# Optimization experiments

Measured on AMD Instinct MI355X. Metric: run time of the kernel, lower is better.

Reference implementation:

```python
import jax, jax.numpy as jnp
import numpy as np
import math

B, S, D, H = 2, 2048, 1024, 16
DK = D // H


def setup_inputs() -> dict:
    key = jax.random.key(0)
    ks = jax.random.split(key, 12)
    std = 1.0 / math.sqrt(D)
    inp = {
        "query": jax.random.normal(ks[0], (B, S, D), jnp.float32),
        "key": jax.random.normal(ks[1], (B, S, D), jnp.float32),
        "value": jax.random.normal(ks[2], (B, S, D), jnp.float32),
        # causal mask, broadcast over batch and heads
        "mask": jnp.tril(jnp.ones((S, S), jnp.int32))[None, None, :, :],
        # nn.Linear weights are [out_features, in_features]
        "Wq": jax.random.uniform(ks[3], (D, D), jnp.float32, -std, std),
        "bq": jax.random.uniform(ks[4], (D,), jnp.float32, -std, std),
        "Wk": jax.random.uniform(ks[5], (D, D), jnp.float32, -std, std),
        "bk": jax.random.uniform(ks[6], (D,), jnp.float32, -std, std),
        "Wv": jax.random.uniform(ks[7], (D, D), jnp.float32, -std, std),
        "bv": jax.random.uniform(ks[8], (D,), jnp.float32, -std, std),
        "Wo": jax.random.uniform(ks[9], (D, D), jnp.float32, -std, std),
        "bo": jax.random.uniform(ks[10], (D,), jnp.float32, -std, std),
    }
    return inp


def reference(query, key, value, mask, Wq, bq, Wk, bk, Wv, bv, Wo, bo):
    q = query @ Wq.T + bq  # [B,S,D]
    k = key @ Wk.T + bk
    v = value @ Wv.T + bv
    # Faithful to the original: a raw view (reshape), NOT a head-transpose split.
    q = q.reshape(B, H, S, DK)
    k = k.reshape(B, H, S, DK)
    v = v.reshape(B, H, S, DK)
    scores = jnp.einsum("bhqd,bhkd->bhqk", q, k) / math.sqrt(DK)
    scores = jnp.where(mask == 0, jnp.float32(-1e9), scores)
    weights = jax.nn.softmax(scores, axis=-1)
    # dropout(p=0.1) is identity in eval mode
    context = jnp.einsum("bhqk,bhkd->bhqd", weights, v)
    context = context.transpose(0, 2, 1, 3).reshape(B, S, D)
    return context @ Wo.T + bo
```

## Files before the change

### kernel.cpp

```cpp
#include <hip/hip_runtime.h>
#include <hip/hip_bf16.h>

#define BB 2
#define SS 2048
#define DD 1024
#define HH 16
#define DKK 64

typedef __attribute__((ext_vector_type(4))) float  f32x4;
typedef __attribute__((ext_vector_type(8))) short  s16x8;
typedef __attribute__((ext_vector_type(4))) short  s16x4;
typedef __attribute__((ext_vector_type(4))) float  fvec4;

__device__ __forceinline__ short f2bs(float f) {
    union { __hip_bfloat16 b; short s; } u;
    u.b = __float2bfloat16(f);
    return u.s;
}

__device__ __forceinline__ void gload_lds16(const short* g, short* l) {
    __builtin_amdgcn_global_load_lds((const __attribute__((address_space(1))) void*)g,
                                     (__attribute__((address_space(3))) void*)l, 16, 0, 0);
}

__global__ __launch_bounds__(256) void cvt_all(
    const float* __restrict__ q,  const float* __restrict__ k,  const float* __restrict__ v,
    const float* __restrict__ wq, const float* __restrict__ wk, const float* __restrict__ wv,
    const float* __restrict__ wo,
    short* __restrict__ qo,  short* __restrict__ ko,  short* __restrict__ vo,
    short* __restrict__ wqo, short* __restrict__ wko, short* __restrict__ wvo,
    short* __restrict__ woo)
{
    const float* src; short* dst; int n;
    switch (blockIdx.y) {
        case 0: src = q;  dst = qo;  n = BB * SS * DD; break;
        case 1: src = k;  dst = ko;  n = BB * SS * DD; break;
        case 2: src = v;  dst = vo;  n = BB * SS * DD; break;
        case 3: src = wq; dst = wqo; n = DD * DD; break;
        case 4: src = wk; dst = wko; n = DD * DD; break;
        case 5: src = wv; dst = wvo; n = DD * DD; break;
        default: src = wo; dst = woo; n = DD * DD; break;
    }
    int i = (blockIdx.x * 256 + threadIdx.x) * 8;
    const int stride = gridDim.x * 256 * 8;
    for (; i < n; i += stride) {
        fvec4 a = *(const fvec4*)&src[i];
        fvec4 b = *(const fvec4*)&src[i + 4];
        s16x8 o;
        o[0] = f2bs(a[0]); o[1] = f2bs(a[1]); o[2] = f2bs(a[2]); o[3] = f2bs(a[3]);
        o[4] = f2bs(b[0]); o[5] = f2bs(b[1]); o[6] = f2bs(b[2]); o[7] = f2bs(b[3]);
        *(s16x8*)&dst[i] = o;
    }
}

template<bool OUTF32>
__global__ __launch_bounds__(256) void gemm_nt_v2(
    const short* __restrict__ A0, const short* __restrict__ A1, const short* __restrict__ A2,
    const short* __restrict__ B0, const short* __restrict__ B1, const short* __restrict__ B2,
    const float* __restrict__ c0, const float* __restrict__ c1, const float* __restrict__ c2,
    void* __restrict__ O0, void* __restrict__ O1, void* __restrict__ O2,
    float os0, float os1, float os2,
    int ko0, int ko1, int ko2,
    int ppx, int NY, int KL, int N, int K)
{
    const int d   = blockIdx.x;
    const int xcd = d & 7;
    const int s   = d >> 3;
    const int x   = s & 7;
    const int pl  = s >> 3;
    const int panel = xcd * ppx + pl;
    const int y   = panel % NY;
    const int z   = panel / NY;

    const short* A    = z == 0 ? A0 : (z == 1 ? A1 : A2);
    const short* Bw   = z == 0 ? B0 : (z == 1 ? B1 : B2);
    const float* bias = z == 0 ? c0 : (z == 1 ? c1 : c2);
    void* Cp          = z == 0 ? O0 : (z == 1 ? O1 : O2);
    const float oscale = z == 0 ? os0 : (z == 1 ? os1 : os2);
    const int koff     = z == 0 ? ko0 : (z == 1 ? ko1 : ko2);

    __shared__ short As[128][64];
    __shared__ short Bs[128][64];

    const int tid  = threadIdx.x;
    const int lane = tid & 63;
    const int wid  = tid >> 6;
    const int r16  = lane & 15;
    const int g    = lane >> 4;
    const int m0   = y * 128;
    const int n0   = x * 128;
    const int wr   = (wid >> 1) * 64;
    const int wc   = (wid & 1) * 64;
    const int srow8 = lane >> 3;
    const int c8    = lane & 7;

    f32x4 acc[4][4];
#pragma unroll
    for (int mi = 0; mi < 4; ++mi)
#pragma unroll
        for (int ni = 0; ni < 4; ++ni) acc[mi][ni] = (f32x4){0.f, 0.f, 0.f, 0.f};

    const int csrc = (c8 ^ srow8) * 8;
    const int nk = KL >> 6;
#pragma unroll 1
    for (int kt = 0; kt < nk; ++kt) {
        const int k0 = koff + kt * 64;
        if (kt) __syncthreads();
#pragma unroll
        for (int q = 0; q < 4; ++q) {
            const int r = wid * 32 + q * 8 + srow8;
            gload_lds16(&A[(size_t)(m0 + r) * K + k0 + csrc], &As[wid * 32 + q * 8][0]);
        }
#pragma unroll
        for (int q = 0; q < 4; ++q) {
            const int r = wid * 32 + q * 8 + srow8;
            gload_lds16(&Bw[(size_t)(n0 + r) * K + k0 + csrc], &Bs[wid * 32 + q * 8][0]);
        }
        __syncthreads();

#pragma unroll
        for (int kk = 0; kk < 2; ++kk) {
            s16x8 af[4], bf[4];
#pragma unroll
            for (int mi = 0; mi < 4; ++mi) {
                const int row = wr + mi * 16 + r16;
                af[mi] = *(const s16x8*)&As[row][((kk * 4 + g) ^ (row & 7)) * 8];
            }
#pragma unroll
            for (int ni = 0; ni < 4; ++ni) {
                const int row = wc + ni * 16 + r16;
                bf[ni] = *(const s16x8*)&Bs[row][((kk * 4 + g) ^ (row & 7)) * 8];
            }
#pragma unroll
            for (int mi = 0; mi < 4; ++mi)
#pragma unroll
                for (int ni = 0; ni < 4; ++ni)
                    acc[mi][ni] = __builtin_amdgcn_mfma_f32_16x16x32_bf16(
                        af[mi], bf[ni], acc[mi][ni], 0, 0, 0);
        }
    }

#pragma unroll
    for (int ni = 0; ni < 4; ++ni) {
        const int col = n0 + wc + ni * 16 + r16;
        const float bv = bias ? bias[col] : 0.f;
#pragma unroll
        for (int mi = 0; mi < 4; ++mi) {
#pragma unroll
            for (int r = 0; r < 4; ++r) {
                const int row = m0 + wr + mi * 16 + g * 4 + r;
                const float vv = (acc[mi][ni][r] + bv) * oscale;
                if constexpr (OUTF32)
                    ((float*)Cp)[(size_t)row * N + col] = vv;
                else
                    ((short*)Cp)[(size_t)row * N + col] = f2bs(vv);
            }
        }
    }
}

__global__ __launch_bounds__(256) void combine_o(
    const float* __restrict__ P0, const float* __restrict__ P1,
    const float* __restrict__ bo, float* __restrict__ out)
{
    const int n = BB * SS * DD;
    int i = (blockIdx.x * 256 + threadIdx.x) * 8;
    const int stride = gridDim.x * 256 * 8;
    for (; i < n; i += stride) {
        fvec4 a0 = *(const fvec4*)&P0[i];
        fvec4 a1 = *(const fvec4*)&P0[i + 4];
        fvec4 b0 = *(const fvec4*)&P1[i];
        fvec4 b1 = *(const fvec4*)&P1[i + 4];
        fvec4 c0 = *(const fvec4*)&bo[i & (DD - 1)];
        fvec4 c1 = *(const fvec4*)&bo[(i + 4) & (DD - 1)];
        fvec4 o0 = a0 + b0 + c0;
        fvec4 o1 = a1 + b1 + c1;
        *(fvec4*)&out[i] = o0;
        *(fvec4*)&out[i + 4] = o1;
    }
}

__global__ __launch_bounds__(256) void mha_transpose_v(
    const short* __restrict__ vp, short* __restrict__ vT)
{
    const int st = blockIdx.x;
    const int bh = blockIdx.y;
    const short* src = vp + (size_t)bh * SS * DKK;
    short*       dst = vT + (size_t)bh * SS * DKK;
    const int tid = threadIdx.x;
#pragma unroll
    for (int i = 0; i < 2; ++i) {
        const int c  = tid + i * 256;
        const int dk = c >> 3;
        const int sc = c & 7;
        const int s0 = st * 64 + sc * 8;
        s16x8 v;
#pragma unroll
        for (int j = 0; j < 8; ++j) v[j] = src[(size_t)(s0 + j) * DKK + dk];
        *(s16x8*)&dst[(size_t)dk * SS + s0] = v;
    }
}

__global__ __launch_bounds__(256, 2) void mha_attn(
    const short* __restrict__ qp, const short* __restrict__ kp,
    const short* __restrict__ vT, short* __restrict__ ctx)
{
    __shared__ short Ks[64][64];
    __shared__ short Vs[64][64];
    __shared__ short P[4][16][72];

    const int tid  = threadIdx.x;
    const int wid  = tid >> 6;
    const int lane = tid & 63;
    const int r16  = lane & 15;
    const int g    = lane >> 4;

    const int bh  = blockIdx.x;
    const int bxp = blockIdx.y;
    const int b   = bh >> 4;
    const int h   = bh & 15;

    const short* Qh = qp + (size_t)bh * SS * DKK;
    const short* Kh = kp + (size_t)bh * SS * DKK;
    const short* Vh = vT + (size_t)bh * SS * DKK;

    const int srow = lane >> 3;
    const int r0   = wid * 16;

#pragma unroll 1
    for (int t = 0; t < 2; ++t) {
        const int grp = t ? (31 - bxp) : bxp;
        const int qr0 = grp * 64 + wid * 16;
        const int nkt = grp + 1;

        const s16x8 qf0 = *(const s16x8*)&Qh[(size_t)(qr0 + r16) * DKK + g * 8];
        const s16x8 qf1 = *(const s16x8*)&Qh[(size_t)(qr0 + r16) * DKK + 32 + g * 8];

        f32x4 po[4];
#pragma unroll
        for (int i = 0; i < 4; ++i) po[i] = (f32x4){0.f, 0.f, 0.f, 0.f};
        float l_[4] = {0.f, 0.f, 0.f, 0.f};

#pragma unroll 1
        for (int j = 0; j < nkt; ++j) {
            const int k0 = j * 64;
            __syncthreads();
            {
                const int rowA = r0 + srow;
                const int rowB = rowA + 8;
                const int cA = (((lane & 7) ^ (rowA & 7)) & 7) * 8;
                const int cB = (((lane & 7) ^ (rowB & 7)) & 7) * 8;
                gload_lds16(&Kh[(size_t)(k0 + rowA) * DKK + cA], &Ks[r0][0]);
                gload_lds16(&Kh[(size_t)(k0 + rowB) * DKK + cB], &Ks[r0 + 8][0]);
                gload_lds16(&Vh[(size_t)rowA * SS + k0 + cA], &Vs[r0][0]);
                gload_lds16(&Vh[(size_t)rowB * SS + k0 + cB], &Vs[r0 + 8][0]);
            }
            __syncthreads();

            f32x4 sc[4];
            __builtin_amdgcn_s_setprio(1);
#pragma unroll
            for (int cg = 0; cg < 4; ++cg) {
                const int R  = cg * 16 + r16;
                const int sw = R & 7;
                const s16x8 kf0 = *(const s16x8*)&Ks[R][((g ^ sw) & 7) * 8];
                const s16x8 kf1 = *(const s16x8*)&Ks[R][(((4 + g) ^ sw) & 7) * 8];
                f32x4 tt = (f32x4){0.f, 0.f, 0.f, 0.f};
                tt = __builtin_amdgcn_mfma_f32_16x16x32_bf16(qf0, kf0, tt, 0, 0, 0);
                tt = __builtin_amdgcn_mfma_f32_16x16x32_bf16(qf1, kf1, tt, 0, 0, 0);
                sc[cg] = tt;
            }
            __builtin_amdgcn_s_setprio(0);

            if (j == nkt - 1) {
#pragma unroll
                for (int cg = 0; cg < 4; ++cg)
#pragma unroll
                    for (int r = 0; r < 4; ++r)
                        if (k0 + cg * 16 + r16 > qr0 + g * 4 + r) sc[cg][r] = -1e9f;
            }
#pragma unroll
            for (int cg = 0; cg < 4; ++cg)
#pragma unroll
                for (int r = 0; r < 4; ++r) {
                    const float p = __expf(sc[cg][r]);
                    l_[r] += p;
                    P[wid][g * 4 + r][cg * 16 + r16] = f2bs(p);
                }
            const s16x8 pf0 = *(const s16x8*)&P[wid][r16][g * 8];
            const s16x8 pf1 = *(const s16x8*)&P[wid][r16][32 + g * 8];

            __builtin_amdgcn_s_setprio(1);
#pragma unroll
            for (int dg = 0; dg < 4; ++dg) {
                const int Rv = dg * 16 + r16;
                const int sw = Rv & 7;
                const s16x8 vf0 = *(const s16x8*)&Vs[Rv][((g ^ sw) & 7) * 8];
                const s16x8 vf1 = *(const s16x8*)&Vs[Rv][(((4 + g) ^ sw) & 7) * 8];
                po[dg] = __builtin_amdgcn_mfma_f32_16x16x32_bf16(pf0, vf0, po[dg], 0, 0, 0);
                po[dg] = __builtin_amdgcn_mfma_f32_16x16x32_bf16(pf1, vf1, po[dg], 0, 0, 0);
            }
            __builtin_amdgcn_s_setprio(0);
        }

#pragma unroll
        for (int r = 0; r < 4; ++r) {
#pragma unroll
            for (int off = 1; off < 16; off <<= 1)
                l_[r] += __shfl_xor(l_[r], off);
        }
#pragma unroll
        for (int dg = 0; dg < 4; ++dg)
#pragma unroll
            for (int r = 0; r < 4; ++r) {
                const int srw = qr0 + g * 4 + r;
                const float v = po[dg][r] * __builtin_amdgcn_rcpf(l_[r]);
                ctx[((size_t)(b * SS + srw)) * DD + h * 64 + dg * 16 + r16] = f2bs(v);
            }
    }
}

extern "C" void kernel_launch(void* const* d_in, const int* in_sizes, int n_in,
                              void* d_out, int out_size, void* d_ws, size_t ws_size,
                              hipStream_t stream) {
    const float* query = (const float*)d_in[0];
    const float* key   = (const float*)d_in[1];
    const float* value = (const float*)d_in[2];
    const float* Wq = (const float*)d_in[4];
    const float* bq = (const float*)d_in[5];
    const float* Wk = (const float*)d_in[6];
    const float* bk = (const float*)d_in[7];
    const float* Wv = (const float*)d_in[8];
    const float* bv = (const float*)d_in[9];
    const float* Wo = (const float*)d_in[10];
    const float* bo = (const float*)d_in[11];
    float* out = (float*)d_out;

    const size_t elems = (size_t)BB * SS * DD;
    const size_t wel   = (size_t)DD * DD;
    short* qx  = (short*)d_ws;
    short* kx  = qx + elems;
    short* vx  = kx + elems;
    short* wqx = vx + elems;
    short* wkx = wqx + wel;
    short* wvx = wkx + wel;
    short* wox = wvx + wel;
    short* qp  = wox + wel;
    short* kp  = qp + elems;
    short* vp  = kp + elems;
    short* vT  = qx;
    short* ctx = vx;
    float* P0  = (float*)qx;
    float* P1  = (float*)qp;

    const int M = BB * SS;

    cvt_all<<<dim3(1024, 7), 256, 0, stream>>>(query, key, value, Wq, Wk, Wv, Wo,
                                               qx, kx, vx, wqx, wkx, wvx, wox);
    gemm_nt_v2<false><<<dim3(768), 256, 0, stream>>>(
        qx, kx, vx, wqx, wkx, wvx, bq, bk, bv, qp, kp, vp,
        0.125f, 1.0f, 1.0f, 0, 0, 0, 12, 32, 1024, DD, DD);
    mha_transpose_v<<<dim3(SS / 64, BB * HH), 256, 0, stream>>>(vp, vT);
    mha_attn<<<dim3(BB * HH, 16), 256, 0, stream>>>(qp, kp, vT, ctx);
    gemm_nt_v2<true><<<dim3(512), 256, 0, stream>>>(
        ctx, ctx, ctx, wox, wox, wox, nullptr, nullptr, nullptr,
        (void*)P0, (void*)P1, (void*)P1,
        1.0f, 1.0f, 1.0f, 0, 512, 512, 8, 32, 512, DD, DD);
    combine_o<<<dim3(2048), 256, 0, stream>>>(P0, P1, bo, out);
}
```

Before: 128.5 us.

## Double-buffer K/V tiles in attention and drop split-K output projection

The attention kernel now stages the next K/V tile into a second LDS buffer while the current tile is computed, using explicit vmcnt waits and raw barriers in place of the load-then-sync pattern. The output projection moves from a split-K GEMM with fp32 partials plus a combine kernel to a single full-K GEMM with a 128x64 tile that adds the bias and writes the output directly. This removes one kernel launch and the traffic for the fp32 partials, and it hides global load latency in attention. The cost is twice the LDS for K/V, which can lower occupancy, and hand-written waitcnt logic that depends on how many loads are in flight.

```diff
diff --git a/kernel.cpp b/kernel.cpp
--- a/kernel.cpp
+++ b/kernel.cpp
@@ -53,21 +53,20 @@
     }
 }
 
-template<bool OUTF32>
+template<int BN, int NXSH, bool OUTF32>
 __global__ __launch_bounds__(256) void gemm_nt_v2(
     const short* __restrict__ A0, const short* __restrict__ A1, const short* __restrict__ A2,
     const short* __restrict__ B0, const short* __restrict__ B1, const short* __restrict__ B2,
     const float* __restrict__ c0, const float* __restrict__ c1, const float* __restrict__ c2,
     void* __restrict__ O0, void* __restrict__ O1, void* __restrict__ O2,
     float os0, float os1, float os2,
-    int ko0, int ko1, int ko2,
     int ppx, int NY, int KL, int N, int K)
 {
     const int d   = blockIdx.x;
     const int xcd = d & 7;
     const int s   = d >> 3;
-    const int x   = s & 7;
-    const int pl  = s >> 3;
+    const int x   = s & ((1 << NXSH) - 1);
+    const int pl  = s >> NXSH;
     const int panel = xcd * ppx + pl;
     const int y   = panel % NY;
     const int z   = panel / NY;
@@ -77,10 +76,9 @@
     const float* bias = z == 0 ? c0 : (z == 1 ? c1 : c2);
     void* Cp          = z == 0 ? O0 : (z == 1 ? O1 : O2);
     const float oscale = z == 0 ? os0 : (z == 1 ? os1 : os2);
-    const int koff     = z == 0 ? ko0 : (z == 1 ? ko1 : ko2);
 
     __shared__ short As[128][64];
-    __shared__ short Bs[128][64];
+    __shared__ short Bs[BN][64];
 
     const int tid  = threadIdx.x;
     const int lane = tid & 63;
@@ -88,23 +86,25 @@
     const int r16  = lane & 15;
     const int g    = lane >> 4;
     const int m0   = y * 128;
-    const int n0   = x * 128;
+    const int n0   = x * BN;
+    constexpr int MR = 4;
+    constexpr int NR = BN / 32;
     const int wr   = (wid >> 1) * 64;
-    const int wc   = (wid & 1) * 64;
+    const int wc   = (wid & 1) * (BN / 2);
     const int srow8 = lane >> 3;
     const int c8    = lane & 7;
 
-    f32x4 acc[4][4];
-#pragma unroll
-    for (int mi = 0; mi < 4; ++mi)
-#pragma unroll
-        for (int ni = 0; ni < 4; ++ni) acc[mi][ni] = (f32x4){0.f, 0.f, 0.f, 0.f};
+    f32x4 acc[MR][NR];
+#pragma unroll
+    for (int mi = 0; mi < MR; ++mi)
+#pragma unroll
+        for (int ni = 0; ni < NR; ++ni) acc[mi][ni] = (f32x4){0.f, 0.f, 0.f, 0.f};
 
     const int csrc = (c8 ^ srow8) * 8;
     const int nk = KL >> 6;
 #pragma unroll 1
     for (int kt = 0; kt < nk; ++kt) {
-        const int k0 = koff + kt * 64;
+        const int k0 = kt * 64;
         if (kt) __syncthreads();
 #pragma unroll
         for (int q = 0; q < 4; ++q) {
@@ -112,40 +112,40 @@
             gload_lds16(&A[(size_t)(m0 + r) * K + k0 + csrc], &As[wid * 32 + q * 8][0]);
         }
 #pragma unroll
-        for (int q = 0; q < 4; ++q) {
-            const int r = wid * 32 + q * 8 + srow8;
-            gload_lds16(&Bw[(size_t)(n0 + r) * K + k0 + csrc], &Bs[wid * 32 + q * 8][0]);
+        for (int q = 0; q < BN / 32; ++q) {
+            const int r = wid * (BN / 4) + q * 8 + srow8;
+            gload_lds16(&Bw[(size_t)(n0 + r) * K + k0 + csrc], &Bs[wid * (BN / 4) + q * 8][0]);
         }
         __syncthreads();
 
 #pragma unroll
         for (int kk = 0; kk < 2; ++kk) {
-            s16x8 af[4], bf[4];
-#pragma unroll
-            for (int mi = 0; mi < 4; ++mi) {
+            s16x8 af[MR], bf[NR];
+#pragma unroll
+            for (int mi = 0; mi < MR; ++mi) {
                 const int row = wr + mi * 16 + r16;
                 af[mi] = *(const s16x8*)&As[row][((kk * 4 + g) ^ (row & 7)) * 8];
             }
 #pragma unroll
-            for (int ni = 0; ni < 4; ++ni) {
+            for (int ni = 0; ni < NR; ++ni) {
                 const int row = wc + ni * 16 + r16;
                 bf[ni] = *(const s16x8*)&Bs[row][((kk * 4 + g) ^ (row & 7)) * 8];
             }
 #pragma unroll
-            for (int mi = 0; mi < 4; ++mi)
-#pragma unroll
-                for (int ni = 0; ni < 4; ++ni)
+            for (int mi = 0; mi < MR; ++mi)
+#pragma unroll
+                for (int ni = 0; ni < NR; ++ni)
                     acc[mi][ni] = __builtin_amdgcn_mfma_f32_16x16x32_bf16(
                         af[mi], bf[ni], acc[mi][ni], 0, 0, 0);
         }
     }
 
 #pragma unroll
-    for (int ni = 0; ni < 4; ++ni) {
+    for (int ni = 0; ni < NR; ++ni) {
         const int col = n0 + wc + ni * 16 + r16;
         const float bv = bias ? bias[col] : 0.f;
 #pragma unroll
-        for (int mi = 0; mi < 4; ++mi) {
+        for (int mi = 0; mi < MR; ++mi) {
 #pragma unroll
             for (int r = 0; r < 4; ++r) {
                 const int row = m0 + wr + mi * 16 + g * 4 + r;
@@ -156,27 +156,6 @@
                     ((short*)Cp)[(size_t)row * N + col] = f2bs(vv);
             }
         }
-    }
-}
-
-__global__ __launch_bounds__(256) void combine_o(
-    const float* __restrict__ P0, const float* __restrict__ P1,
-    const float* __restrict__ bo, float* __restrict__ out)
-{
-    const int n = BB * SS * DD;
-    int i = (blockIdx.x * 256 + threadIdx.x) * 8;
-    const int stride = gridDim.x * 256 * 8;
-    for (; i < n; i += stride) {
-        fvec4 a0 = *(const fvec4*)&P0[i];
-        fvec4 a1 = *(const fvec4*)&P0[i + 4];
-        fvec4 b0 = *(const fvec4*)&P1[i];
-        fvec4 b1 = *(const fvec4*)&P1[i + 4];
-        fvec4 c0 = *(const fvec4*)&bo[i & (DD - 1)];
-        fvec4 c1 = *(const fvec4*)&bo[(i + 4) & (DD - 1)];
-        fvec4 o0 = a0 + b0 + c0;
-        fvec4 o1 = a1 + b1 + c1;
-        *(fvec4*)&out[i] = o0;
-        *(fvec4*)&out[i + 4] = o1;
     }
 }
 
@@ -205,8 +184,8 @@
     const short* __restrict__ qp, const short* __restrict__ kp,
     const short* __restrict__ vT, short* __restrict__ ctx)
 {
-    __shared__ short Ks[64][64];
-    __shared__ short Vs[64][64];
+    __shared__ short Ks[2][64][64];
+    __shared__ short Vs[2][64][64];
     __shared__ short P[4][16][72];
 
     const int tid  = threadIdx.x;
@@ -225,7 +204,18 @@
     const short* Vh = vT + (size_t)bh * SS * DKK;
 
     const int srow = lane >> 3;
+    const int csw  = (((lane & 7) ^ srow) & 7) * 8;
     const int r0   = wid * 16;
+
+    auto STAGE = [&](int buf, int j) {
+        const int k0 = j * 64;
+        const int rA = r0 + srow;
+        const int rB = rA + 8;
+        gload_lds16(&Kh[(size_t)(k0 + rA) * DKK + csw], &Ks[buf][r0][0]);
+        gload_lds16(&Kh[(size_t)(k0 + rB) * DKK + csw], &Ks[buf][r0 + 8][0]);
+        gload_lds16(&Vh[(size_t)rA * SS + k0 + csw],    &Vs[buf][r0][0]);
+        gload_lds16(&Vh[(size_t)rB * SS + k0 + csw],    &Vs[buf][r0 + 8][0]);
+    };
 
 #pragma unroll 1
     for (int t = 0; t < 2; ++t) {
@@ -241,21 +231,20 @@
         for (int i = 0; i < 4; ++i) po[i] = (f32x4){0.f, 0.f, 0.f, 0.f};
         float l_[4] = {0.f, 0.f, 0.f, 0.f};
 
+        STAGE(0, 0);
+
 #pragma unroll 1
         for (int j = 0; j < nkt; ++j) {
+            const int cur = j & 1;
             const int k0 = j * 64;
-            __syncthreads();
-            {
-                const int rowA = r0 + srow;
-                const int rowB = rowA + 8;
-                const int cA = (((lane & 7) ^ (rowA & 7)) & 7) * 8;
-                const int cB = (((lane & 7) ^ (rowB & 7)) & 7) * 8;
-                gload_lds16(&Kh[(size_t)(k0 + rowA) * DKK + cA], &Ks[r0][0]);
-                gload_lds16(&Kh[(size_t)(k0 + rowB) * DKK + cB], &Ks[r0 + 8][0]);
-                gload_lds16(&Vh[(size_t)rowA * SS + k0 + cA], &Vs[r0][0]);
-                gload_lds16(&Vh[(size_t)rowB * SS + k0 + cB], &Vs[r0 + 8][0]);
-            }
-            __syncthreads();
+            if (j + 1 < nkt) {
+                STAGE(cur ^ 1, j + 1);
+                asm volatile("s_waitcnt vmcnt(4)" ::: "memory");
+            } else {
+                asm volatile("s_waitcnt vmcnt(0)" ::: "memory");
+            }
+            __builtin_amdgcn_s_barrier();
+            __builtin_amdgcn_sched_barrier(0);
 
             f32x4 sc[4];
             __builtin_amdgcn_s_setprio(1);
@@ -263,8 +252,8 @@
             for (int cg = 0; cg < 4; ++cg) {
                 const int R  = cg * 16 + r16;
                 const int sw = R & 7;
-                const s16x8 kf0 = *(const s16x8*)&Ks[R][((g ^ sw) & 7) * 8];
-                const s16x8 kf1 = *(const s16x8*)&Ks[R][(((4 + g) ^ sw) & 7) * 8];
+                const s16x8 kf0 = *(const s16x8*)&Ks[cur][R][((g ^ sw) & 7) * 8];
+                const s16x8 kf1 = *(const s16x8*)&Ks[cur][R][(((4 + g) ^ sw) & 7) * 8];
                 f32x4 tt = (f32x4){0.f, 0.f, 0.f, 0.f};
                 tt = __builtin_amdgcn_mfma_f32_16x16x32_bf16(qf0, kf0, tt, 0, 0, 0);
                 tt = __builtin_amdgcn_mfma_f32_16x16x32_bf16(qf1, kf1, tt, 0, 0, 0);
@@ -295,12 +284,16 @@
             for (int dg = 0; dg < 4; ++dg) {
                 const int Rv = dg * 16 + r16;
                 const int sw = Rv & 7;
-                const s16x8 vf0 = *(const s16x8*)&Vs[Rv][((g ^ sw) & 7) * 8];
-                const s16x8 vf1 = *(const s16x8*)&Vs[Rv][(((4 + g) ^ sw) & 7) * 8];
+                const s16x8 vf0 = *(const s16x8*)&Vs[cur][Rv][((g ^ sw) & 7) * 8];
+                const s16x8 vf1 = *(const s16x8*)&Vs[cur][Rv][(((4 + g) ^ sw) & 7) * 8];
                 po[dg] = __builtin_amdgcn_mfma_f32_16x16x32_bf16(pf0, vf0, po[dg], 0, 0, 0);
                 po[dg] = __builtin_amdgcn_mfma_f32_16x16x32_bf16(pf1, vf1, po[dg], 0, 0, 0);
             }
             __builtin_amdgcn_s_setprio(0);
+
+            __builtin_amdgcn_sched_barrier(0);
+            asm volatile("s_waitcnt lgkmcnt(0)" ::: "memory");
+            __builtin_amdgcn_s_barrier();
         }
 
 #pragma unroll
@@ -350,21 +343,15 @@
     short* vp  = kp + elems;
     short* vT  = qx;
     short* ctx = vx;
-    float* P0  = (float*)qx;
-    float* P1  = (float*)qp;
-
-    const int M = BB * SS;
 
     cvt_all<<<dim3(1024, 7), 256, 0, stream>>>(query, key, value, Wq, Wk, Wv, Wo,
                                                qx, kx, vx, wqx, wkx, wvx, wox);
-    gemm_nt_v2<false><<<dim3(768), 256, 0, stream>>>(
+    gemm_nt_v2<128, 3, false><<<dim3(768), 256, 0, stream>>>(
         qx, kx, vx, wqx, wkx, wvx, bq, bk, bv, qp, kp, vp,
-        0.125f, 1.0f, 1.0f, 0, 0, 0, 12, 32, 1024, DD, DD);
+        0.125f, 1.0f, 1.0f, 12, 32, 1024, DD, DD);
     mha_transpose_v<<<dim3(SS / 64, BB * HH), 256, 0, stream>>>(vp, vT);
     mha_attn<<<dim3(BB * HH, 16), 256, 0, stream>>>(qp, kp, vT, ctx);
-    gemm_nt_v2<true><<<dim3(512), 256, 0, stream>>>(
-        ctx, ctx, ctx, wox, wox, wox, nullptr, nullptr, nullptr,
-        (void*)P0, (void*)P1, (void*)P1,
-        1.0f, 1.0f, 1.0f, 0, 512, 512, 8, 32, 512, DD, DD);
-    combine_o<<<dim3(2048), 256, 0, stream>>>(P0, P1, bo, out);
-}
+    gemm_nt_v2<64, 4, true><<<dim3(512), 256, 0, stream>>>(
+        ctx, ctx, ctx, wox, wox, wox, bo, bo, bo, out, out, out,
+        1.0f, 1.0f, 1.0f, 4, 32, 1024, DD, DD);
+}
```

Measured after the change: 121.2 us. -5.7%, faster.
